# Performance work log

Measured on AMD Instinct MI355X. Metric: run time of the kernel, lower is better.

Reference implementation:

```python
import jax, jax.numpy as jnp
from jax import lax
import numpy as np

D = 256   # d_model
NL = 5    # n_levels
NH = 8    # n_heads
NP = 4    # n_points
DH = D // NH
D_FFN = 1024


def conv2d(x, w, b, stride=1, pad=0):
    y = lax.conv_general_dilated(x, w, (stride, stride), ((pad, pad), (pad, pad)),
                                 dimension_numbers=('NCHW', 'OIHW', 'NCHW'))
    return y + b[None, :, None, None]


def groupnorm(x, g, b, groups=32, eps=1e-5):
    N, C, H, W = x.shape
    xr = x.reshape(N, groups, C // groups, H, W)
    mu = xr.mean((2, 3, 4), keepdims=True)
    var = xr.var((2, 3, 4), keepdims=True)
    xr = (xr - mu) / jnp.sqrt(var + eps)
    return xr.reshape(N, C, H, W) * g[None, :, None, None] + b[None, :, None, None]


def layernorm(x, g, b, eps=1e-5):
    mu = x.mean(-1, keepdims=True)
    var = x.var(-1, keepdims=True)
    return (x - mu) / jnp.sqrt(var + eps) * g + b


def bilinear_sample(value_l, loc, H, W):
    # value_l: (N, H*W, NH, DH); loc: (N, Lq, NH, NP, 2) normalized to [0,1]
    # matches F.grid_sample(mode='bilinear', padding_mode='zeros', align_corners=False)
    N, Lq, nH, nP, _ = loc.shape
    dh = value_l.shape[-1]
    x = loc[..., 0] * W - 0.5
    y = loc[..., 1] * H - 0.5
    x0 = jnp.floor(x)
    y0 = jnp.floor(y)
    wx = x - x0
    wy = y - y0
    x0i = x0.astype(jnp.int32)
    y0i = y0.astype(jnp.int32)
    vt = value_l.transpose(0, 2, 1, 3)  # (N, NH, HW, DH)

    def corner(ix, iy, w):
        valid = (ix >= 0) & (ix < W) & (iy >= 0) & (iy < H)
        idx = jnp.clip(iy, 0, H - 1) * W + jnp.clip(ix, 0, W - 1)  # (N,Lq,NH,NP)
        idx_t = idx.transpose(0, 2, 1, 3).reshape(N, nH, Lq * nP)
        v = jnp.take_along_axis(vt, idx_t[..., None], axis=2)  # (N,NH,Lq*NP,DH)
        v = v.reshape(N, nH, Lq, nP, dh).transpose(0, 2, 1, 3, 4)
        return v * (w * valid)[..., None]

    return (corner(x0i, y0i, (1 - wx) * (1 - wy))
            + corner(x0i + 1, y0i, wx * (1 - wy))
            + corner(x0i, y0i + 1, (1 - wx) * wy)
            + corner(x0i + 1, y0i + 1, wx * wy))


def msdeform_attn(query, ref_pts, value_in, shapes,
                  W_off, b_off, W_aw, b_aw, W_val, b_val, W_out, b_out):
    N, Lq, _ = query.shape
    value = (value_in @ W_val.T + b_val).reshape(N, -1, NH, DH)
    off = (query @ W_off.T + b_off).reshape(N, Lq, NH, NL, NP, 2)
    aw = jax.nn.softmax((query @ W_aw.T + b_aw).reshape(N, Lq, NH, NL * NP), axis=-1)
    aw = aw.reshape(N, Lq, NH, NL, NP)
    # offset normalizer is (W, H) per level
    norm = jnp.array([[wl, hl] for (hl, wl) in shapes], jnp.float32)
    loc = ref_pts[:, :, None, :, None, :] + off / norm[None, None, None, :, None, :]
    out = jnp.zeros((N, Lq, NH, DH), query.dtype)
    start = 0
    for l, (hl, wl) in enumerate(shapes):
        v = value[:, start:start + hl * wl]
        start += hl * wl
        s = bilinear_sample(v, loc[:, :, :, l], hl, wl)  # (N,Lq,NH,NP,DH)
        out = out + jnp.einsum('nqhpd,nqhp->nqhd', s, aw[:, :, :, l])
    return out.reshape(N, Lq, D) @ W_out.T + b_out


def setup_inputs():
    ks = iter(jax.random.split(jax.random.key(0), 48))
    def nrm(shape, s=1.0):
        return jax.random.normal(next(ks), shape, jnp.float32) * s
    return {
        'x0': nrm((2, 128, 100, 100)),
        'x1': nrm((2, 256, 50, 50)),
        'x2': nrm((2, 512, 25, 25)),
        'x3': nrm((2, 1024, 13, 13)),
        'W_ref': nrm((NL * 2, D), 0.02), 'b_ref': jnp.zeros((NL * 2,), jnp.float32),
        'W_off': nrm((NH * NL * NP * 2, D), 0.02), 'b_off': jnp.zeros((NH * NL * NP * 2,), jnp.float32),
        'W_aw': nrm((NH * NL * NP, D), 0.02), 'b_aw': jnp.zeros((NH * NL * NP,), jnp.float32),
        'W_val': nrm((D, D), 0.02), 'b_val': jnp.zeros((D,), jnp.float32),
        'W_out': nrm((D, D), 0.02), 'b_out': jnp.zeros((D,), jnp.float32),
        'gn_g': jnp.ones((D,), jnp.float32), 'gn_b': jnp.zeros((D,), jnp.float32),
        'Wc1': nrm((256, 128, 1, 1), 0.05), 'bc1': jnp.zeros((256,), jnp.float32),
        'Wc2': nrm((256, 512, 1, 1), 0.05), 'bc2': jnp.zeros((256,), jnp.float32),
        'Wc3': nrm((256, 1024, 1, 1), 0.05), 'bc3': jnp.zeros((256,), jnp.float32),
        'Wc4': nrm((256, 1024, 3, 3), 0.02), 'bc4': jnp.zeros((256,), jnp.float32),
        'Wc11': nrm((128, 256, 1, 1), 0.05), 'bc11': jnp.zeros((128,), jnp.float32),
        'Wc22': nrm((512, 256, 1, 1), 0.05), 'bc22': jnp.zeros((512,), jnp.float32),
        'Wc33': nrm((1024, 256, 1, 1), 0.05), 'bc33': jnp.zeros((1024,), jnp.float32),
        'ln1_g': jnp.ones((D,), jnp.float32), 'ln1_b': jnp.zeros((D,), jnp.float32),
        'W1': nrm((D_FFN, D), 0.02), 'b1f': jnp.zeros((D_FFN,), jnp.float32),
        'W2': nrm((D, D_FFN), 0.02), 'b2f': jnp.zeros((D,), jnp.float32),
        'ln2_g': jnp.ones((D,), jnp.float32), 'ln2_b': jnp.zeros((D,), jnp.float32),
    }


def reference(x0, x1, x2, x3, W_ref, b_ref, W_off, b_off, W_aw, b_aw,
              W_val, b_val, W_out, b_out, gn_g, gn_b,
              Wc1, bc1, Wc2, bc2, Wc3, bc3, Wc4, bc4,
              Wc11, bc11, Wc22, bc22, Wc33, bc33,
              ln1_g, ln1_b, W1, b1f, W2, b2f, ln2_g, ln2_b):
    # eval mode: all dropouts are identity
    srcs = [groupnorm(conv2d(x0, Wc1, bc1), gn_g, gn_b),
            x1,
            groupnorm(conv2d(x2, Wc2, bc2), gn_g, gn_b),
            groupnorm(conv2d(x3, Wc3, bc3), gn_g, gn_b),
            groupnorm(conv2d(x3, Wc4, bc4, stride=2, pad=1), gn_g, gn_b)]
    shapes = [(int(s.shape[2]), int(s.shape[3])) for s in srcs]
    N = x0.shape[0]
    src = jnp.concatenate([s.reshape(N, D, -1).transpose(0, 2, 1) for s in srcs], axis=1)
    L = src.shape[1]
    ref_pts = jax.nn.sigmoid(src @ W_ref.T + b_ref).reshape(N, L, NL, 2)
    attn = msdeform_attn(src, ref_pts, src, shapes,
                         W_off, b_off, W_aw, b_aw, W_val, b_val, W_out, b_out)
    h = layernorm(src + attn, ln1_g, ln1_b)
    ffn = jax.nn.relu(h @ W1.T + b1f) @ W2.T + b2f
    h = layernorm(h + ffn, ln2_g, ln2_b)
    sizes = [hl * wl for (hl, wl) in shapes]
    parts = jnp.split(h, np.cumsum(sizes)[:-1].tolist(), axis=1)
    feats = [p.transpose(0, 2, 1).reshape(N, D, hl, wl) for p, (hl, wl) in zip(parts, shapes)]
    return (conv2d(feats[0], Wc11, bc11), feats[1],
            conv2d(feats[2], Wc22, bc22), conv2d(feats[3], Wc33, bc33))
```

## Files before the change

kernel.cpp:

```cpp
#include <hip/hip_runtime.h>
#include <hip/hip_bf16.h>
#include <hip/hip_fp16.h>

#define LTOT 13343
#define NLQ  26686
#define WS_VALB 27326464
#define WS_R    122969088
#define WS_AW   (WS_R + 17079040)
#define WS_REF  (WS_R + 25618560)

typedef __attribute__((ext_vector_type(8))) short bf16x8;
typedef __attribute__((ext_vector_type(4))) float f32x4;
typedef _Float16 f16x2 __attribute__((ext_vector_type(2)));

__device__ __forceinline__ short f2bs(float x) {
  __hip_bfloat16 h = __float2bfloat16(x);
  return __builtin_bit_cast(short, h);
}
__device__ __forceinline__ float b2f(__hip_bfloat16 x) { return __bfloat162float(x); }
__device__ __forceinline__ unsigned short f2bu(float x) {
  return __builtin_bit_cast(unsigned short, __float2bfloat16(x));
}

__device__ __forceinline__ void gld16(const void* g, void* l) {
  __builtin_amdgcn_global_load_lds(
      (const __attribute__((address_space(1))) void*)g,
      (__attribute__((address_space(3))) void*)l, 16, 0, 0);
}

template<int MT, int AMODE, int EPI, int WMODE>
__global__ __launch_bounds__(256) void mgemm_k(
    const __hip_bfloat16* __restrict__ A, const void* __restrict__ Wv,
    const float* __restrict__ bias, void* __restrict__ outv,
    const __hip_bfloat16* __restrict__ resid,
    const float* __restrict__ lng, const float* __restrict__ lnb,
    int M, int Nc, int K, int k_len,
    int A_HW, int A_L, int A_off,
    int O_HW, int O_L, int O_off)
{
  constexpr int NT = (EPI == 9) ? 256 : 128;
  constexpr int JF = (MT == 128 || EPI == 9) ? 4 : 2;
  constexpr bool FAST = (AMODE == 0 && WMODE == 0);
  constexpr int AK = FAST ? 64 : 32;
  constexpr int PA = MT * 32;
  constexpr int PB = NT * 32;
  __shared__ __hip_bfloat16 ldsA[MT * AK];
  __shared__ __hip_bfloat16 ldsB[NT * AK];
  const int t = threadIdx.x;
  const int bm = blockIdx.x * MT, bn = blockIdx.y * NT;
  const int k0 = blockIdx.z * k_len;

  const int sl = t & 63;
  const int mloc = sl & 15;
  const int kbase = (sl >> 4) * 8;
  const int s0 = t >> 6;

  const int r0 = bm + s0 * 16 + mloc, r1 = r0 + 64;
  const int nc0 = bn + s0 * 16 + mloc, nc1 = nc0 + 64;
  const int nc2 = nc0 + 128, nc3 = nc0 + 192;

  const __hip_bfloat16 *ap0 = A, *ap1 = A;
  bool av0 = false, av1 = false;
  int g0n=0, g0h=0, g0w=0, g1n=0, g1h=0, g1w=0;
  if (AMODE == 0) {
    if (r0 < M) { int nn = r0 / A_HW, p = r0 - nn * A_HW;
      ap0 = A + (size_t)(nn * A_L + A_off + p) * K + kbase; av0 = true; }
    if (MT == 128 && r1 < M) { int nn = r1 / A_HW, p = r1 - nn * A_HW;
      ap1 = A + (size_t)(nn * A_L + A_off + p) * K + kbase; av1 = true; }
  } else {
    if (r0 < M) { g0n = r0 / 49; int p = r0 - g0n * 49; g0h = p / 7; g0w = p - g0h * 7; av0 = true; }
    if (r1 < M) { g1n = r1 / 49; int p = r1 - g1n * 49; g1h = p / 7; g1w = p - g1h * 7; av1 = true; }
  }
  const bool wv0 = nc0 < Nc, wv1 = nc1 < Nc;
  const bool wv2 = (EPI == 9) && (nc2 < Nc), wv3 = (EPI == 9) && (nc3 < Nc);
  const __hip_bfloat16 *wb0 = (const __hip_bfloat16*)Wv, *wb1 = wb0, *wb2 = wb0, *wb3 = wb0;
  const float *wf0 = (const float*)Wv, *wf1 = wf0;
  if (WMODE == 0) {
    if (wv0) wb0 = (const __hip_bfloat16*)Wv + (size_t)nc0 * K + kbase;
    if (wv1) wb1 = (const __hip_bfloat16*)Wv + (size_t)nc1 * K + kbase;
    if (wv2) wb2 = (const __hip_bfloat16*)Wv + (size_t)nc2 * K + kbase;
    if (wv3) wb3 = (const __hip_bfloat16*)Wv + (size_t)nc3 * K + kbase;
  } else {
    if (wv0) wf0 = (const float*)Wv + (size_t)nc0 * 9216;
    if (wv1) wf1 = (const float*)Wv + (size_t)nc1 * 9216;
  }

  __hip_bfloat16* lbA0 = ldsA + s0 * 512;
  __hip_bfloat16* lbA1 = lbA0 + 2048;
  __hip_bfloat16* lbB0 = ldsB + s0 * 512;
  __hip_bfloat16* lbB1 = lbB0 + 2048;
  __hip_bfloat16* lbB2 = lbB0 + 4096;
  __hip_bfloat16* lbB3 = lbB0 + 6144;
  __hip_bfloat16* lwA0 = ldsA + s0 * 512 + sl * 8;
  __hip_bfloat16* lwA1 = lwA0 + 2048;
  __hip_bfloat16* lwB0 = ldsB + s0 * 512 + sl * 8;
  __hip_bfloat16* lwB1 = lwB0 + 2048;

  const int lane = t & 63, wv_ = t >> 6;
  const __hip_bfloat16 *rA, *rB;
  int wmR, colbase;
  if (MT == 128) {
    int wm = wv_ >> 1, wn = wv_ & 1;
    rA = ldsA + wm * 2048 + lane * 8;
    rB = ldsB + wn * 2048 + lane * 8;
    wmR = wm * 64;
    colbase = bn + wn * 64;
  } else if (EPI == 9) {
    rA = ldsA + lane * 8;
    rB = ldsB + wv_ * 2048 + lane * 8;
    wmR = 0;
    colbase = bn + wv_ * 64;
  } else {
    rA = ldsA + lane * 8;
    rB = ldsB + wv_ * 1024 + lane * 8;
    wmR = 0;
    colbase = bn + wv_ * 32;
  }

  f32x4 acc[4][JF] = {};

  if (FAST) {
    for (int kt = k0; kt < k0 + k_len; kt += 64) {
      if (av0) { gld16(ap0 + kt, lbA0); gld16(ap0 + kt + 32, lbA0 + PA); }
      if (MT == 128) {
        if (av1) { gld16(ap1 + kt, lbA1); gld16(ap1 + kt + 32, lbA1 + PA); }
      }
      if (wv0) { gld16(wb0 + kt, lbB0); gld16(wb0 + kt + 32, lbB0 + PB); }
      if (wv1) { gld16(wb1 + kt, lbB1); gld16(wb1 + kt + 32, lbB1 + PB); }
      if (EPI == 9) {
        if (wv2) { gld16(wb2 + kt, lbB2); gld16(wb2 + kt + 32, lbB2 + PB); }
        if (wv3) { gld16(wb3 + kt, lbB3); gld16(wb3 + kt + 32, lbB3 + PB); }
      }
      __syncthreads();
#pragma unroll
      for (int h = 0; h < 2; h++) {
        bf16x8 af[4], bfr[JF];
#pragma unroll
        for (int i = 0; i < 4; i++) af[i] = *(const bf16x8*)(rA + h * PA + i * 512);
#pragma unroll
        for (int j = 0; j < JF; j++) bfr[j] = *(const bf16x8*)(rB + h * PB + j * 512);
#pragma unroll
        for (int i = 0; i < 4; i++)
#pragma unroll
          for (int j = 0; j < JF; j++)
            acc[i][j] = __builtin_amdgcn_mfma_f32_16x16x32_bf16(af[i], bfr[j], acc[i][j], 0, 0, 0);
      }
      __syncthreads();
    }
  } else {
    for (int kt = k0; kt < k0 + k_len; kt += 32) {
      {
        bf16x8 va0 = {}, va1 = {};
        int kp = kt + kbase;
        int rs = kp >> 10, c = kp & 1023;
        int rr = rs / 3, ss = rs - rr * 3;
        if (av0) { int ih = g0h*2-1+rr, iw = g0w*2-1+ss;
          if ((unsigned)ih < 13u && (unsigned)iw < 13u)
            va0 = *(const bf16x8*)(A + ((size_t)(g0n*169 + ih*13 + iw))*1024 + c); }
        if (av1) { int ih = g1h*2-1+rr, iw = g1w*2-1+ss;
          if ((unsigned)ih < 13u && (unsigned)iw < 13u)
            va1 = *(const bf16x8*)(A + ((size_t)(g1n*169 + ih*13 + iw))*1024 + c); }
        *(bf16x8*)lwA0 = va0;  *(bf16x8*)lwA1 = va1;
      }
      {
        bf16x8 vb0 = {}, vb1 = {};
        int kp = kt + kbase;
        int rs = kp >> 10, c = kp & 1023;
        if (wv0) { const float* p = wf0 + (size_t)c * 9 + rs;
#pragma unroll
          for (int j = 0; j < 8; j++) vb0[j] = f2bs(p[j * 9]); }
        if (wv1) { const float* p = wf1 + (size_t)c * 9 + rs;
#pragma unroll
          for (int j = 0; j < 8; j++) vb1[j] = f2bs(p[j * 9]); }
        *(bf16x8*)lwB0 = vb0;  *(bf16x8*)lwB1 = vb1;
      }
      __syncthreads();
      bf16x8 af[4], bfr[JF];
#pragma unroll
      for (int i = 0; i < 4; i++) af[i] = *(const bf16x8*)(rA + i * 512);
#pragma unroll
      for (int j = 0; j < JF; j++) bfr[j] = *(const bf16x8*)(rB + j * 512);
#pragma unroll
      for (int i = 0; i < 4; i++)
#pragma unroll
        for (int j = 0; j < JF; j++)
          acc[i][j] = __builtin_amdgcn_mfma_f32_16x16x32_bf16(af[i], bfr[j], acc[i][j], 0, 0, 0);
      __syncthreads();
    }
  }

  const int quad = lane >> 4, nl = lane & 15;

  if constexpr (EPI == 9) {
    float* red  = (float*)ldsB;
    float* redm = (float*)ldsB + 600;
    float bv9[4], gj[4], bj[4]; int cj9[4];
#pragma unroll
    for (int j = 0; j < 4; j++) {
      cj9[j] = colbase + j * 16 + nl;
      bv9[j] = bias[cj9[j]];
      gj[j]  = lng[cj9[j]];
      bj[j]  = lnb[cj9[j]];
    }
#pragma unroll
    for (int i = 0; i < 4; i++) {
#pragma unroll
      for (int r = 0; r < 4; r++) {
        int row64 = i * 16 + quad * 4 + r;
        int m = bm + row64;
        if (m < M) {
          int n = m / O_HW, p = m - n * O_HW;
          size_t orow = (size_t)(n * O_L + O_off + p);
#pragma unroll
          for (int j = 0; j < 4; j++) {
            float v = acc[i][j][r] + bv9[j] + b2f(resid[orow * Nc + cj9[j]]);
            acc[i][j][r] = b2f(__float2bfloat16(v));
          }
        } else {
#pragma unroll
          for (int j = 0; j < 4; j++) acc[i][j][r] = 0.f;
        }
        float s  = acc[i][0][r] + acc[i][1][r] + acc[i][2][r] + acc[i][3][r];
        float s2 = acc[i][0][r]*acc[i][0][r] + acc[i][1][r]*acc[i][1][r]
                 + acc[i][2][r]*acc[i][2][r] + acc[i][3][r]*acc[i][3][r];
        s  += __shfl_xor(s, 1, 64);  s2 += __shfl_xor(s2, 1, 64);
        s  += __shfl_xor(s, 2, 64);  s2 += __shfl_xor(s2, 2, 64);
        s  += __shfl_xor(s, 4, 64);  s2 += __shfl_xor(s2, 4, 64);
        s  += __shfl_xor(s, 8, 64);  s2 += __shfl_xor(s2, 8, 64);
        if (nl == 0) { red[row64 * 9 + wv_ * 2] = s; red[row64 * 9 + wv_ * 2 + 1] = s2; }
      }
    }
    __syncthreads();
    if (t < 64) {
      float S = 0.f, S2 = 0.f;
#pragma unroll
      for (int w = 0; w < 4; w++) { S += red[t * 9 + w * 2]; S2 += red[t * 9 + w * 2 + 1]; }
      float mean = S * (1.f / 256.f);
      float var  = S2 * (1.f / 256.f) - mean * mean;
      redm[t * 2]     = mean;
      redm[t * 2 + 1] = rsqrtf(var + 1e-5f);
    }
    __syncthreads();
#pragma unroll
    for (int i = 0; i < 4; i++) {
#pragma unroll
      for (int r = 0; r < 4; r++) {
        int row64 = i * 16 + quad * 4 + r;
        int m = bm + row64;
        if (m >= M) continue;
        float mean = redm[row64 * 2], rstd = redm[row64 * 2 + 1];
        int n = m / O_HW, p = m - n * O_HW;
        size_t orow = (size_t)(n * O_L + O_off + p);
#pragma unroll
        for (int j = 0; j < 4; j++) {
          float o = (acc[i][j][r] - mean) * rstd * gj[j] + bj[j];
          ((__hip_bfloat16*)outv)[orow * Nc + cj9[j]] = __float2bfloat16(o);
        }
      }
    }
    return;
  }

  float bv[JF]; int cj[JF]; bool cv[JF];
#pragma unroll
  for (int j = 0; j < JF; j++) {
    cj[j] = colbase + j * 16 + nl;
    cv[j] = cj[j] < Nc;
    bv[j] = (EPI != 3 && cv[j]) ? bias[cj[j]] : 0.f;
  }
#pragma unroll
  for (int i = 0; i < 4; i++) {
#pragma unroll
    for (int r = 0; r < 4; r++) {
      int m = bm + wmR + i * 16 + quad * 4 + r;
      if (m >= M) continue;
      int n = m / O_HW, p = m - n * O_HW;
      size_t orow = (size_t)(n * O_L + O_off + p);
#pragma unroll
      for (int j = 0; j < JF; j++) {
        if (!cv[j]) continue;
        float v = acc[i][j][r] + bv[j];
        if (EPI == 1) v = 1.f / (1.f + expf(-v));
        if (EPI == 2) v = fmaxf(v, 0.f);
        if (EPI == 0 || EPI == 1) ((float*)outv)[orow * Nc + cj[j]] = v;
        else if (EPI == 2 || EPI == 6) ((__hip_bfloat16*)outv)[orow * Nc + cj[j]] = __float2bfloat16(v);
        else if (EPI == 3) atomicAdd((float*)outv + orow * Nc + cj[j], acc[i][j][r]);
        else if (EPI == 8) {
          float rv = b2f(resid[orow * Nc + cj[j]]);
          ((__hip_bfloat16*)outv)[orow * Nc + cj[j]] = __float2bfloat16(v + rv);
        }
        else if (EPI == 7) {
          char* base = (char*)outv;
          int q = m, c = cj[j];
          if (c < 256)
            ((_Float16*)(base + WS_VALB))[(size_t)q * 256 + c] = (_Float16)v;
          else if (c < 576)
            ((_Float16*)(base + WS_R))[(size_t)q * 320 + (c - 256)] = (_Float16)v;
          else if (c < 736)
            ((_Float16*)(base + WS_AW))[(size_t)q * 160 + (c - 576)] = (_Float16)v;
          else {
            float sv = 1.f / (1.f + expf(-v));
            ((float*)(base + WS_REF))[(size_t)q * 10 + (c - 736)] = sv;
          }
        }
        else ((float*)outv)[((size_t)n * Nc + cj[j]) * O_HW + p] = v;
      }
    }
  }
}

struct GJob {
  const __hip_bfloat16* A; const __hip_bfloat16* W;
  const float* bias; float* out;
  int M, Nc, K, A_HW, A_L, A_off, O_HW, O_L, O_off, base, nbx;
};
struct GJobs { GJob j[3]; };

template<int EPI, bool WITHCOPY, bool WITHC4>
__global__ __launch_bounds__(256) void mgemm3_k(GJobs tab, int gend,
    const __hip_bfloat16* __restrict__ cpsrc, float* __restrict__ cpdst,
    const __hip_bfloat16* __restrict__ c4A, const __hip_bfloat16* __restrict__ c4W,
    float* __restrict__ c4out, float* __restrict__ stats)
{
  __shared__ char smem[24576];
  __hip_bfloat16* ldsA = (__hip_bfloat16*)smem;
  __hip_bfloat16* ldsB = (__hip_bfloat16*)(smem + 8192);
  const int t = threadIdx.x;
  const int b = blockIdx.x;

  if (WITHCOPY && b >= gend) {
    int bb = b - gend;
    float (*tile)[33] = (float(*)[33])smem;
    int p0 = (bb % 79) * 32; int r = bb / 79; int c0 = (r & 7) * 32; int n = r >> 3;
    int tx = t & 31, ty = t >> 5;
    for (int i = ty; i < 32; i += 8) {
      int p = p0 + i, c = c0 + tx;
      tile[tx][i] = (p < 2500) ? b2f(cpsrc[((size_t)(n * LTOT + 10000 + p)) * 256 + c]) : 0.f;
    }
    __syncthreads();
    for (int i = ty; i < 32; i += 8) {
      int c = c0 + i, p = p0 + tx;
      if (p < 2500) cpdst[((size_t)n * 256 + c) * 2500 + p] = tile[i][tx];
    }
    return;
  }

  if (WITHC4 && b >= gend) {
    int cb = b - gend;
    int kz = cb >> 2, bx2 = cb & 1, by2 = (cb >> 1) & 1;
    int bm = bx2 * 64, bn = by2 * 128;
    int k0 = kz * 288;
    const int sl = t & 63, mloc = sl & 15, kbase = (sl >> 4) * 8, s0 = t >> 6;
    int r0 = bm + s0 * 16 + mloc;
    bool av0 = r0 < 98;
    int g0n = 0, g0h = 0, g0w = 0;
    if (av0) { g0n = r0 / 49; int p = r0 - g0n * 49; g0h = p / 7; g0w = p - g0h * 7; }
    int nc0 = bn + s0 * 16 + mloc, nc1 = nc0 + 64;
    const __hip_bfloat16* wb0 = c4W + (size_t)nc0 * 9216;
    const __hip_bfloat16* wb1 = c4W + (size_t)nc1 * 9216;
    __hip_bfloat16* lwA0 = ldsA + s0 * 512 + sl * 8;
    __hip_bfloat16* lwB0 = ldsB + s0 * 512 + sl * 8;
    __hip_bfloat16* lwB1 = lwB0 + 2048;
    const int lane = t & 63, wvw = t >> 6;
    const __hip_bfloat16* rA = ldsA + lane * 8;
    const __hip_bfloat16* rB = ldsB + wvw * 1024 + lane * 8;
    const int colbase = bn + wvw * 32;
    f32x4 acc[4][2] = {};
    for (int kt = k0; kt < k0 + 288; kt += 32) {
      int kp = kt + kbase;
      {
        bf16x8 va0 = {};
        int rs = kp >> 10, c = kp & 1023;
        int rr = rs / 3, ss = rs - rr * 3;
        if (av0) { int ih = g0h*2-1+rr, iw = g0w*2-1+ss;
          if ((unsigned)ih < 13u && (unsigned)iw < 13u)
            va0 = *(const bf16x8*)(c4A + ((size_t)(g0n*169 + ih*13 + iw))*1024 + c); }
        *(bf16x8*)lwA0 = va0;
      }
      *(bf16x8*)lwB0 = *(const bf16x8*)(wb0 + kp);
      *(bf16x8*)lwB1 = *(const bf16x8*)(wb1 + kp);
      __syncthreads();
      bf16x8 af[4], bfr[2];
#pragma unroll
      for (int i = 0; i < 4; i++) af[i] = *(const bf16x8*)(rA + i * 512);
#pragma unroll
      for (int j2 = 0; j2 < 2; j2++) bfr[j2] = *(const bf16x8*)(rB + j2 * 512);
#pragma unroll
      for (int i = 0; i < 4; i++)
#pragma unroll
        for (int j2 = 0; j2 < 2; j2++)
          acc[i][j2] = __builtin_amdgcn_mfma_f32_16x16x32_bf16(af[i], bfr[j2], acc[i][j2], 0, 0, 0);
      __syncthreads();
    }
    const int quad = lane >> 4, nl = lane & 15;
#pragma unroll
    for (int i = 0; i < 4; i++) {
#pragma unroll
      for (int r = 0; r < 4; r++) {
        int m = bm + i * 16 + quad * 4 + r;
        if (m >= 98) continue;
        int n = m / 49, p = m - n * 49;
        size_t orow = (size_t)(n * LTOT + 13294 + p);
#pragma unroll
        for (int j2 = 0; j2 < 2; j2++)
          atomicAdd(c4out + orow * 256 + colbase + j2 * 16 + nl, acc[i][j2][r]);
      }
    }
    return;
  }

  const int j = (b >= tab.j[1].base) + (b >= tab.j[2].base);
  const GJob J = tab.j[j];
  const int local = b - J.base;
  const int bx = local % J.nbx, by = local / J.nbx;
  const int bm = bx * 64, bn = by * 128;

  const int sl = t & 63, mloc = sl & 15, kbase = (sl >> 4) * 8, s0 = t >> 6;
  const int r0 = bm + s0 * 16 + mloc;
  const int nc0 = bn + s0 * 16 + mloc, nc1 = nc0 + 64;

  const __hip_bfloat16* ap0 = J.A; bool av0 = false;
  if (r0 < J.M) { int nn = r0 / J.A_HW, p = r0 - nn * J.A_HW;
    ap0 = J.A + (size_t)(nn * J.A_L + J.A_off + p) * J.K + kbase; av0 = true; }
  const bool wv0 = nc0 < J.Nc, wv1 = nc1 < J.Nc;
  const __hip_bfloat16 *wb0 = J.W, *wb1 = J.W;
  if (wv0) wb0 = J.W + (size_t)nc0 * J.K + kbase;
  if (wv1) wb1 = J.W + (size_t)nc1 * J.K + kbase;

  __hip_bfloat16* lbA0 = ldsA + s0 * 512;
  __hip_bfloat16* lbB0 = ldsB + s0 * 512;
  __hip_bfloat16* lbB1 = lbB0 + 2048;
  const int lane = t & 63, wv_ = t >> 6;
  const __hip_bfloat16* rA = ldsA + lane * 8;
  const __hip_bfloat16* rB = ldsB + wv_ * 1024 + lane * 8;
  const int colbase = bn + wv_ * 32;

  f32x4 acc[4][2] = {};
  for (int kt = 0; kt < J.K; kt += 64) {
    if (av0) { gld16(ap0 + kt, lbA0); gld16(ap0 + kt + 32, lbA0 + 2048); }
    if (wv0) { gld16(wb0 + kt, lbB0); gld16(wb0 + kt + 32, lbB0 + 4096); }
    if (wv1) { gld16(wb1 + kt, lbB1); gld16(wb1 + kt + 32, lbB1 + 4096); }
    __syncthreads();
#pragma unroll
    for (int h = 0; h < 2; h++) {
      bf16x8 af[4], bfr[2];
#pragma unroll
      for (int i = 0; i < 4; i++) af[i] = *(const bf16x8*)(rA + h * 2048 + i * 512);
#pragma unroll
      for (int j2 = 0; j2 < 2; j2++) bfr[j2] = *(const bf16x8*)(rB + h * 4096 + j2 * 512);
#pragma unroll
      for (int i = 0; i < 4; i++)
#pragma unroll
        for (int j2 = 0; j2 < 2; j2++)
          acc[i][j2] = __builtin_amdgcn_mfma_f32_16x16x32_bf16(af[i], bfr[j2], acc[i][j2], 0, 0, 0);
    }
    __syncthreads();
  }

  const int quad = lane >> 4, nl = lane & 15;
  float bv[2]; int cj[2];
#pragma unroll
  for (int j2 = 0; j2 < 2; j2++) {
    cj[j2] = colbase + j2 * 16 + nl;
    bv[j2] = J.bias[cj[j2]];
  }

  if constexpr (EPI == 0) {
    float sA[2] = {0.f, 0.f}, qA[2] = {0.f, 0.f};
    float sB[2] = {0.f, 0.f}, qB[2] = {0.f, 0.f};
#pragma unroll
    for (int i = 0; i < 4; i++) {
#pragma unroll
      for (int r = 0; r < 4; r++) {
        int m = bm + i * 16 + quad * 4 + r;
        if (m >= J.M) continue;
        int n = m / J.O_HW, p = m - n * J.O_HW;
        size_t orow = (size_t)(n * J.O_L + J.O_off + p);
#pragma unroll
        for (int j2 = 0; j2 < 2; j2++) {
          float v = acc[i][j2][r] + bv[j2];
          J.out[orow * J.Nc + cj[j2]] = v;
          if (n == 0) { sA[j2] += v; qA[j2] += v * v; }
          else        { sB[j2] += v; qB[j2] += v * v; }
        }
      }
    }
    const int msks[5] = {1, 2, 4, 16, 32};
#pragma unroll
    for (int j2 = 0; j2 < 2; j2++) {
      float s0v = sA[j2], q0v = qA[j2], s1v = sB[j2], q1v = qB[j2];
#pragma unroll
      for (int d = 0; d < 5; d++) {
        int msk = msks[d];
        s0v += __shfl_xor(s0v, msk, 64);  q0v += __shfl_xor(q0v, msk, 64);
        s1v += __shfl_xor(s1v, msk, 64);  q1v += __shfl_xor(q1v, msk, 64);
      }
      if (lane == 0 || lane == 8) {
        int g = cj[j2] >> 3;
        if (s0v != 0.f || q0v != 0.f) {
          int si = (j * 2 + 0) * 32 + g;
          atomicAdd(&stats[si * 2], s0v);  atomicAdd(&stats[si * 2 + 1], q0v);
        }
        if (s1v != 0.f || q1v != 0.f) {
          int si = (j * 2 + 1) * 32 + g;
          atomicAdd(&stats[si * 2], s1v);  atomicAdd(&stats[si * 2 + 1], q1v);
        }
      }
    }
    return;
  }

  float* tbuf = (float*)smem;
#pragma unroll
  for (int h2 = 0; h2 < 2; h2++) {
    __syncthreads();
    if ((wv_ >> 1) == h2) {
      int cbase = (wv_ & 1) * 32;
#pragma unroll
      for (int i = 0; i < 4; i++)
#pragma unroll
        for (int r = 0; r < 4; r++) {
          int pl = i * 16 + quad * 4 + r;
#pragma unroll
          for (int j2 = 0; j2 < 2; j2++)
            tbuf[pl * 65 + cbase + j2 * 16 + nl] = acc[i][j2][r] + bv[j2];
        }
    }
    __syncthreads();
#pragma unroll
    for (int kk = 0; kk < 16; kk++) {
      int idx = kk * 256 + t;
      int cl = idx >> 6, pl = idx & 63;
      int m = bm + pl;
      if (m < J.M) {
        int n = m / J.O_HW, p = m - n * J.O_HW;
        J.out[((size_t)n * J.Nc + (bn + h2 * 64 + cl)) * J.O_HW + p] = tbuf[pl * 65 + cl];
      }
    }
  }
}

#define CVT_T13 1632768
struct CvtEnt { const float* s; __hip_bfloat16* d; int n; int base; };
struct CvtTab { CvtEnt e[13]; };
__global__ __launch_bounds__(256) void cvt_weights_k(CvtTab tab,
    const float* __restrict__ bv, const float* __restrict__ bo,
    const float* __restrict__ ba, const float* __restrict__ br,
    float* __restrict__ catbias, float* __restrict__ stats,
    float* __restrict__ src, const float* __restrict__ bc4,
    const float* __restrict__ Wc4f, __hip_bfloat16* __restrict__ wt4)
{
  int i = blockIdx.x * 256 + threadIdx.x;
  if (i < CVT_T13) {
#pragma unroll
    for (int j = 12; j >= 0; j--) {
      if (i >= tab.e[j].base) {
        int k = i - tab.e[j].base;
        tab.e[j].d[k] = __float2bfloat16(tab.e[j].s[k]);
        return;
      }
    }
    return;
  }
  int i2 = i - CVT_T13;
  if (i2 < 1024) {
    if (i2 < 746) {
      float v;
      if (i2 < 256) v = bv[i2];
      else if (i2 < 576) v = bo[i2 - 256];
      else if (i2 < 736) v = ba[i2 - 576];
      else v = br[i2 - 736];
      catbias[i2] = v;
    }
    if (i2 < 512) stats[i2] = 0.f;
    return;
  }
  i2 -= 1024;
  if (i2 < 25088) {
    int blk = i2 >> 8, c = i2 & 255;
    int n = blk / 49, p = blk - n * 49;
    src[((size_t)(n * LTOT + 13294 + p)) * 256 + c] = bc4[c];
    return;
  }
  i2 -= 25088;
  if (i2 < 262144) {
    int nc = i2 >> 10, c = i2 & 1023;
    const float* s = Wc4f + (size_t)nc * 9216 + (size_t)c * 9;
    __hip_bfloat16* d = wt4 + (size_t)nc * 9216 + c;
#pragma unroll
    for (int rs = 0; rs < 9; rs++) d[rs * 1024] = __float2bfloat16(s[rs]);
  }
}

__global__ __launch_bounds__(256) void transpose_all_k(
    const float* __restrict__ x0, const float* __restrict__ x2,
    const float* __restrict__ x3, const float* __restrict__ x1,
    __hip_bfloat16* __restrict__ xt0, __hip_bfloat16* __restrict__ xt2,
    __hip_bfloat16* __restrict__ xt3, __hip_bfloat16* __restrict__ srcb)
{
  __shared__ float tile[32][33];
  int b = blockIdx.x;
  const float* x; __hip_bfloat16* xt; int C, HW, gx, gy, n, lvl1 = 0;
  if (b < 2504)      { x = x0; xt = xt0; C = 128;  HW = 10000; gx = b % 313; int r = b / 313; gy = r & 3; n = r >> 2; }
  else if (b < 3144) { int bb = b - 2504; x = x2; xt = xt2; C = 512;  HW = 625; gx = bb % 20; int r = bb / 20; gy = r & 15; n = r >> 4; }
  else if (b < 3528) { int bb = b - 3144; x = x3; xt = xt3; C = 1024; HW = 169; gx = bb % 6;  int r = bb / 6;  gy = r & 31; n = r >> 5; }
  else               { int bb = b - 3528; x = x1; xt = srcb; C = 256; HW = 2500; gx = bb % 79; int r = bb / 79; gy = r & 7; n = r >> 3; lvl1 = 1; }
  int p0 = gx * 32, c0 = gy * 32;
  const float* xb = x + (size_t)n * C * HW;
  __hip_bfloat16* xtb = lvl1 ? (srcb + ((size_t)(n * LTOT + 10000)) * 256)
                             : (xt + (size_t)n * HW * C);
  int tx = threadIdx.x & 31, ty = threadIdx.x >> 5;
  for (int i = ty; i < 32; i += 8) {
    int c = c0 + i, p = p0 + tx;
    tile[i][tx] = (p < HW) ? xb[(size_t)c * HW + p] : 0.f;
  }
  __syncthreads();
  for (int i = ty; i < 32; i += 8) {
    int p = p0 + i, c = c0 + tx;
    if (p < HW) xtb[(size_t)p * C + c] = __float2bfloat16(tile[tx][i]);
  }
}

__global__ __launch_bounds__(256) void gn_stats4_k(const float* __restrict__ src,
                                                   float* __restrict__ stats)
{
  int n = blockIdx.x, t = threadIdx.x;
  const float* base = src + ((size_t)(n * LTOT + 13294)) * 256 + t;
  float s = 0.f, s2 = 0.f;
  for (int r = 0; r < 49; r++) {
    float v = base[(size_t)r * 256];
    s += v; s2 += v * v;
  }
  s  += __shfl_down(s, 4, 64);  s2 += __shfl_down(s2, 4, 64);
  s  += __shfl_down(s, 2, 64);  s2 += __shfl_down(s2, 2, 64);
  s  += __shfl_down(s, 1, 64);  s2 += __shfl_down(s2, 1, 64);
  if ((t & 7) == 0) {
    int g = t >> 3;
    int si = (3 * 2 + n) * 32 + g;
    atomicAdd(&stats[si * 2],     s);
    atomicAdd(&stats[si * 2 + 1], s2);
  }
}

__global__ __launch_bounds__(256) void gn_apply_k(const float* __restrict__ src,
    __hip_bfloat16* __restrict__ srcb,
    const float* __restrict__ stats, const float* __restrict__ g,
    const float* __restrict__ b)
{
  int x = blockIdx.x;
  int n = x / 10843, cidx = x - n * 10843;
  int li, off, hw, p;
  if (cidx < 10000)      { li = 0; off = 0;     hw = 10000; p = cidx; }
  else if (cidx < 10625) { li = 1; off = 12500; hw = 625;   p = cidx - 10000; }
  else if (cidx < 10794) { li = 2; off = 13125; hw = 169;   p = cidx - 10625; }
  else                   { li = 3; off = 13294; hw = 49;    p = cidx - 10794; }
  int t = threadIdx.x;
  int si = (li * 2 + n) * 32 + (t >> 3);
  float cnt = (float)(hw * 8);
  float mean = stats[si * 2] / cnt;
  float var = stats[si * 2 + 1] / cnt - mean * mean;
  float rstd = rsqrtf(var + 1e-5f);
  size_t a = ((size_t)(n * LTOT + off + p)) * 256 + t;
  float v = (src[a] - mean) * rstd * g[t] + b[t];
  srcb[a] = __float2bfloat16(v);
}

__global__ __launch_bounds__(256) void msdeform_k(const _Float16* __restrict__ value,
    const _Float16* __restrict__ offb, const _Float16* __restrict__ awb,
    const float* __restrict__ refb, __hip_bfloat16* __restrict__ out)
{
  __shared__ float s_awraw[320];
  __shared__ float s_ref[20];
  __shared__ float s_stat[32];
  __shared__ int4 s_cA[320];
  __shared__ int4 s_cB[320];
  const int t = threadIdx.x;
  const int q0 = blockIdx.x * 2;

  for (int i = t; i < 320; i += 256) {
    int ql = (i >= 160) ? 1 : 0;
    s_awraw[i] = (float)awb[(size_t)(q0 + ql) * 160 + (i - ql * 160)];
  }
  if (t < 20) {
    int ql = (t >= 10) ? 1 : 0;
    s_ref[t] = refb[(size_t)(q0 + ql) * 10 + (t - ql * 10)];
  }
  __syncthreads();

  if (t < 16) {
    const float* p = s_awraw + t * 20;
    float m = p[0];
#pragma unroll
    for (int j = 1; j < 20; j++) m = fmaxf(m, p[j]);
    float s = 0.f;
#pragma unroll
    for (int j = 0; j < 20; j++) s += expf(p[j] - m);
    s_stat[t * 2] = m;
    s_stat[t * 2 + 1] = 1.f / s;
  }
  __syncthreads();

  {
    const int Wl[5]   = {100, 50, 25, 13, 7};
    const int lvlo[5] = {0, 10000, 12500, 13125, 13294};
    for (int i = t; i < 320; i += 256) {
      int ql = (i >= 160) ? 1 : 0;
      int j = i - ql * 160;
      int h = j / 20, pt = j - h * 20;
      int l = pt >> 2;
      int q = q0 + ql;
      int W = Wl[l], lo = lvlo[l];
      float fW = (float)W;
      f16x2 o2h = *(const f16x2*)(offb + (size_t)q * 320 + j * 2);
      float ox = (float)o2h[0], oy = (float)o2h[1];
      int hs = (ql * 8 + h) * 2;
      float wgt = expf(s_awraw[i] - s_stat[hs]) * s_stat[hs + 1];
      float rx = s_ref[ql * 10 + l * 2], ry = s_ref[ql * 10 + l * 2 + 1];
      float x = (rx + ox / fW) * fW - 0.5f;
      float y = (ry + oy / fW) * fW - 0.5f;
      float x0f = floorf(x), y0f = floorf(y);
      float wx = x - x0f, wy = y - y0f;
      int x0 = (int)x0f, y0 = (int)y0f;
      int hb = h * 64;
      auto mk = [&](int ix, int iy, float w) {
        bool v = (ix >= 0) & (ix < W) & (iy >= 0) & (iy < W);
        int cx = min(max(ix, 0), W - 1), cy = min(max(iy, 0), W - 1);
        int off = (lo + cy * W + cx) * 512 + hb;
        float fw = v ? w * wgt : 0.f;
        unsigned hbits = (unsigned)__builtin_bit_cast(unsigned short, (_Float16)fw);
        return make_int2(off, (int)(hbits | (hbits << 16)));
      };
      int2 c00 = mk(x0,     y0,     (1.f - wx) * (1.f - wy));
      int2 c10 = mk(x0 + 1, y0,     wx * (1.f - wy));
      int2 c01 = mk(x0,     y0 + 1, (1.f - wx) * wy);
      int2 c11 = mk(x0 + 1, y0 + 1, wx * wy);
      s_cA[i] = make_int4(c00.x, c00.y, c10.x, c10.y);
      s_cB[i] = make_int4(c01.x, c01.y, c11.x, c11.y);
    }
  }
  __syncthreads();

  const int ql = t >> 7, h = (t >> 4) & 7, c2 = t & 15;
  const int q = q0 + ql;
  const int n = q / LTOT;
  const char* vb = (const char*)value + (size_t)n * LTOT * 512 + c2 * 4;
  f16x2 accA = {0, 0}, accB = {0, 0};
  const int bi = ql * 160 + h * 20;
#pragma unroll 5
  for (int p = 0; p < 20; p++) {
    int4 A = s_cA[bi + p];
    int4 B = s_cB[bi + p];
    {
      f16x2 v2 = __builtin_bit_cast(f16x2, *(const unsigned*)(vb + A.x));
      f16x2 w2 = __builtin_bit_cast(f16x2, (unsigned)A.y);
      accA = w2 * v2 + accA;
    }
    {
      f16x2 v2 = __builtin_bit_cast(f16x2, *(const unsigned*)(vb + A.z));
      f16x2 w2 = __builtin_bit_cast(f16x2, (unsigned)A.w);
      accB = w2 * v2 + accB;
    }
    {
      f16x2 v2 = __builtin_bit_cast(f16x2, *(const unsigned*)(vb + B.x));
      f16x2 w2 = __builtin_bit_cast(f16x2, (unsigned)B.y);
      accA = w2 * v2 + accA;
    }
    {
      f16x2 v2 = __builtin_bit_cast(f16x2, *(const unsigned*)(vb + B.z));
      f16x2 w2 = __builtin_bit_cast(f16x2, (unsigned)B.w);
      accB = w2 * v2 + accB;
    }
  }
  float a0 = (float)accA[0] + (float)accB[0];
  float a1 = (float)accA[1] + (float)accB[1];
  unsigned o0 = (unsigned)f2bu(a0);
  unsigned o1 = (unsigned)f2bu(a1);
  *(unsigned*)((char*)out + ((size_t)q * 256 + h * 32 + c2 * 2) * 2) = (o1 << 16) | o0;
}

extern "C" void kernel_launch(void* const* d_in, const int* in_sizes, int n_in,
                              void* d_out, int out_size, void* d_ws, size_t ws_size,
                              hipStream_t stream)
{
  const float* x0    = (const float*)d_in[0];
  const float* x1    = (const float*)d_in[1];
  const float* x2    = (const float*)d_in[2];
  const float* x3    = (const float*)d_in[3];
  const float* W_ref = (const float*)d_in[4];
  const float* b_ref = (const float*)d_in[5];
  const float* W_off = (const float*)d_in[6];
  const float* b_off = (const float*)d_in[7];
  const float* W_aw  = (const float*)d_in[8];
  const float* b_aw  = (const float*)d_in[9];
  const float* W_val = (const float*)d_in[10];
  const float* b_val = (const float*)d_in[11];
  const float* W_outp= (const float*)d_in[12];
  const float* b_outp= (const float*)d_in[13];
  const float* gn_g  = (const float*)d_in[14];
  const float* gn_b  = (const float*)d_in[15];
  const float* Wc1   = (const float*)d_in[16];
  const float* bc1   = (const float*)d_in[17];
  const float* Wc2   = (const float*)d_in[18];
  const float* bc2   = (const float*)d_in[19];
  const float* Wc3   = (const float*)d_in[20];
  const float* bc3   = (const float*)d_in[21];
  const float* Wc4   = (const float*)d_in[22];
  const float* bc4   = (const float*)d_in[23];
  const float* Wc11  = (const float*)d_in[24];
  const float* bc11  = (const float*)d_in[25];
  const float* Wc22  = (const float*)d_in[26];
  const float* bc22  = (const float*)d_in[27];
  const float* Wc33  = (const float*)d_in[28];
  const float* bc33  = (const float*)d_in[29];
  const float* ln1_g = (const float*)d_in[30];
  const float* ln1_b = (const float*)d_in[31];
  const float* W1    = (const float*)d_in[32];
  const float* b1f   = (const float*)d_in[33];
  const float* W2    = (const float*)d_in[34];
  const float* b2f_  = (const float*)d_in[35];
  const float* ln2_g = (const float*)d_in[36];
  const float* ln2_b = (const float*)d_in[37];

  char* wsb = (char*)d_ws;
  float* src             = (float*)(wsb + 0);
  _Float16* valb         = (_Float16*)(wsb + WS_VALB);
  __hip_bfloat16* h2b    = (__hip_bfloat16*)(wsb + 54652928);
  __hip_bfloat16* srcb   = (__hip_bfloat16*)(wsb + 81979392);
  __hip_bfloat16* h1b    = (__hip_bfloat16*)(wsb + 95642624);
  __hip_bfloat16* sampb  = (__hip_bfloat16*)(wsb + 109305856);
  __hip_bfloat16* midb   = (__hip_bfloat16*)(wsb + WS_R);
  _Float16* offbh        = (_Float16*)(wsb + WS_R);
  _Float16* awbh         = (_Float16*)(wsb + WS_AW);
  float* refb            = (float*)(wsb + WS_REF);
  __hip_bfloat16* xt0    = (__hip_bfloat16*)(wsb + WS_R);
  __hip_bfloat16* xt2    = (__hip_bfloat16*)(wsb + WS_R + 5120000);
  __hip_bfloat16* xt3    = (__hip_bfloat16*)(wsb + WS_R + 6400000);
  __hip_bfloat16* wWc4t  = (__hip_bfloat16*)(wsb + WS_R + 8388608);
  __hip_bfloat16* warena = (__hip_bfloat16*)(wsb + 177622016);
  float* stats           = (float*)(wsb + 180887552);
  float* catbias         = (float*)(wsb + 180889600);
  const size_t needed = 180892672;
  if (ws_size < needed) return;

  __hip_bfloat16* wWproj = warena + 0;
  __hip_bfloat16* wW_val = warena + 0;
  __hip_bfloat16* wW_off = warena + 65536;
  __hip_bfloat16* wW_aw  = warena + 147456;
  __hip_bfloat16* wW_ref = warena + 188416;
  __hip_bfloat16* wW_out = warena + 190976;
  __hip_bfloat16* wW1    = warena + 256512;
  __hip_bfloat16* wW2    = warena + 518656;
  __hip_bfloat16* wWc1   = warena + 780800;
  __hip_bfloat16* wWc2   = warena + 813568;
  __hip_bfloat16* wWc3   = warena + 944640;
  __hip_bfloat16* wWc11  = warena + 1206784;
  __hip_bfloat16* wWc22  = warena + 1239552;
  __hip_bfloat16* wWc33  = warena + 1370624;

  dim3 B(256);

  CvtTab tab = {{
    {W_val, wW_val, 65536, 0},       {W_off, wW_off, 81920, 65536},
    {W_aw,  wW_aw,  40960, 147456},  {W_ref, wW_ref, 2560,  188416},
    {W_outp,wW_out, 65536, 190976},  {W1,    wW1,  262144,  256512},
    {W2,    wW2,  262144,  518656},  {Wc1,   wWc1,  32768,  780800},
    {Wc2,   wWc2, 131072,  813568},  {Wc3,   wWc3, 262144,  944640},
    {Wc11,  wWc11, 32768, 1206784},  {Wc22,  wWc22,131072, 1239552},
    {Wc33,  wWc33,262144, 1370624}
  }};
  cvt_weights_k<<<7504,B,0,stream>>>(tab, b_val, b_off, b_aw, b_ref,
                                     catbias, stats, src, bc4, Wc4, wWc4t);

  transpose_all_k<<<4792,B,0,stream>>>(x0, x2, x3, x1, xt0, xt2, xt3, srcb);

  GJobs injobs = {{
    { xt0, wWc1, bc1, src, 20000, 256, 128,  20000, 0, 0, 10000, LTOT, 0,     0,   313 },
    { xt2, wWc2, bc2, src, 1250,  256, 512,  1250,  0, 0, 625,   LTOT, 12500, 626, 20  },
    { xt3, wWc3, bc3, src, 338,   256, 1024, 338,   0, 0, 169,   LTOT, 13125, 666, 6   }
  }};
  mgemm3_k<0,false,true><<<806,B,0,stream>>>(injobs, 678, nullptr, nullptr,
                                             xt3, wWc4t, src, stats);
  gn_stats4_k<<<2,B,0,stream>>>(src, stats);
  gn_apply_k<<<21686,B,0,stream>>>(src, srcb, stats, gn_g, gn_b);

  mgemm_k<128,0,7,0><<<dim3(209,6),B,0,stream>>>(srcb, wWproj, catbias, d_ws, nullptr, nullptr, nullptr, NLQ,746,256,256, NLQ,0,0, NLQ,0,0);
  msdeform_k<<<13343,B,0,stream>>>(valb, offbh, awbh, refb, sampb);

  mgemm_k<64,0,9,0><<<dim3(417,1),B,0,stream>>>(sampb, wW_out, b_outp, h1b, srcb, ln1_g, ln1_b, NLQ,256,256,256, NLQ,0,0, NLQ,0,0);

  mgemm_k<128,0,2,0><<<dim3(209,8),B,0,stream>>>(h1b,  wW1, b1f,  midb,  nullptr, nullptr, nullptr, NLQ,1024,256,256, NLQ,0,0, NLQ,0,0);
  mgemm_k<64,0,9,0><<<dim3(417,1), B,0,stream>>>(midb, wW2, b2f_, h2b, h1b, ln2_g, ln2_b, NLQ,256,1024,1024, NLQ,0,0, NLQ,0,0);

  float* out = (float*)d_out;
  GJobs outjobs = {{
    { h2b, wWc11, bc11, out,           20000, 128,  256, 10000, LTOT, 0,     10000, 0, 0, 0,   313 },
    { h2b, wWc22, bc22, out + 3840000, 1250,  512,  256, 625,   LTOT, 12500, 625,   0, 0, 313, 20  },
    { h2b, wWc33, bc33, out + 4480000, 338,   1024, 256, 169,   LTOT, 13125, 169,   0, 0, 393, 6   }
  }};
  mgemm3_k<4,true,false><<<1705,B,0,stream>>>(outjobs, 441, h2b, out + 2560000,
                                              nullptr, nullptr, nullptr, nullptr);
}
```

Before: 497.4 us.

## Fuse FFN GEMMs, ReLU, residual and LayerNorm into one kernel

Replaces the two FFN GEMM launches with a single kernel. Each 64-row block keeps its h1 tile in LDS and computes the 1024-wide hidden activation in 128-column chunks held in LDS. Each chunk is multiplied immediately by the matching W2 slice, and the kernel finishes with bias, residual and LayerNorm. This removes the global write and read of the large intermediate activation and one launch. In exchange it uses 64KB of LDS per block with only 417 blocks, so occupancy is low, and weight loads are synchronous with no double buffering.

```diff
diff --git a/kernel.cpp b/kernel.cpp
--- a/kernel.cpp
+++ b/kernel.cpp
@@ -304,6 +304,176 @@
           }
         }
         else ((float*)outv)[((size_t)n * Nc + cj[j]) * O_HW + p] = v;
+      }
+    }
+  }
+}
+
+__global__ __launch_bounds__(256) void ffn_k(
+    const __hip_bfloat16* __restrict__ h1, const __hip_bfloat16* __restrict__ W1,
+    const float* __restrict__ b1, const __hip_bfloat16* __restrict__ W2,
+    const float* __restrict__ b2, const float* __restrict__ lng,
+    const float* __restrict__ lnb, __hip_bfloat16* __restrict__ out)
+{
+  __shared__ char smem[65536];
+  __hip_bfloat16* ldsA = (__hip_bfloat16*)smem;
+  __hip_bfloat16* ldsM = (__hip_bfloat16*)(smem + 32768);
+  __hip_bfloat16* ldsW = (__hip_bfloat16*)(smem + 49152);
+  const int t = threadIdx.x;
+  const int bm = blockIdx.x * 64;
+  const int sl = t & 63, mloc = sl & 15, kbase = (sl >> 4) * 8, s0 = t >> 6;
+  const int lane = t & 63, wv_ = t >> 6;
+  const int quad = lane >> 4, nl = lane & 15;
+
+  const int r0 = bm + s0 * 16 + mloc;
+  if (r0 < NLQ) {
+    const __hip_bfloat16* ap = h1 + (size_t)r0 * 256 + kbase;
+#pragma unroll
+    for (int p = 0; p < 4; p++) {
+      gld16(ap + p * 64,      ldsA + p * 4096 + s0 * 512);
+      gld16(ap + p * 64 + 32, ldsA + p * 4096 + s0 * 512 + 2048);
+    }
+  }
+
+  const int ca = s0 * 16 + mloc;
+  const __hip_bfloat16* rA = ldsA + lane * 8;
+  const __hip_bfloat16* rM = ldsM + lane * 8;
+  const __hip_bfloat16* rB = ldsW + wv_ * 1024 + lane * 8;
+
+  f32x4 acc2[4][4] = {};
+
+  for (int c = 0; c < 8; c++) {
+    f32x4 acc1[4][2] = {};
+    const __hip_bfloat16* wp0 = W1 + (size_t)(c * 128 + ca) * 256 + kbase;
+    const __hip_bfloat16* wp1 = wp0 + (size_t)64 * 256;
+    for (int kt = 0; kt < 256; kt += 64) {
+      gld16(wp0 + kt,      ldsW + s0 * 512);
+      gld16(wp0 + kt + 32, ldsW + s0 * 512 + 4096);
+      gld16(wp1 + kt,      ldsW + s0 * 512 + 2048);
+      gld16(wp1 + kt + 32, ldsW + s0 * 512 + 2048 + 4096);
+      __syncthreads();
+      const int p = kt >> 6;
+#pragma unroll
+      for (int h = 0; h < 2; h++) {
+        bf16x8 af[4], bfr[2];
+#pragma unroll
+        for (int i = 0; i < 4; i++) af[i] = *(const bf16x8*)(rA + p * 4096 + h * 2048 + i * 512);
+#pragma unroll
+        for (int j = 0; j < 2; j++) bfr[j] = *(const bf16x8*)(rB + h * 4096 + j * 512);
+#pragma unroll
+        for (int i = 0; i < 4; i++)
+#pragma unroll
+          for (int j = 0; j < 2; j++)
+            acc1[i][j] = __builtin_amdgcn_mfma_f32_16x16x32_bf16(af[i], bfr[j], acc1[i][j], 0, 0, 0);
+      }
+      __syncthreads();
+    }
+#pragma unroll
+    for (int j = 0; j < 2; j++) {
+      int kc = wv_ * 32 + j * 16 + nl;
+      float bb = b1[c * 128 + kc];
+      int ka = (kc >> 6) * 4096 + ((kc >> 5) & 1) * 2048 + ((kc >> 3) & 3) * 128 + (kc & 7);
+#pragma unroll
+      for (int i = 0; i < 4; i++)
+#pragma unroll
+        for (int r = 0; r < 4; r++) {
+          float v = fmaxf(acc1[i][j][r] + bb, 0.f);
+          ldsM[ka + i * 512 + (quad * 4 + r) * 8] = __float2bfloat16(v);
+        }
+    }
+    for (int kt2 = 0; kt2 < 128; kt2 += 64) {
+      const int p2 = kt2 >> 6;
+#pragma unroll
+      for (int hc = 0; hc < 2; hc++) {
+        const __hip_bfloat16* wq0 = W2 + (size_t)(hc * 128 + ca) * 1024 + c * 128 + kt2 + kbase;
+        const __hip_bfloat16* wq1 = wq0 + (size_t)64 * 1024;
+        gld16(wq0,      ldsW + s0 * 512);
+        gld16(wq0 + 32, ldsW + s0 * 512 + 4096);
+        gld16(wq1,      ldsW + s0 * 512 + 2048);
+        gld16(wq1 + 32, ldsW + s0 * 512 + 2048 + 4096);
+        __syncthreads();
+#pragma unroll
+        for (int h = 0; h < 2; h++) {
+          bf16x8 mf[4], bfr[2];
+#pragma unroll
+          for (int i = 0; i < 4; i++) mf[i] = *(const bf16x8*)(rM + p2 * 4096 + h * 2048 + i * 512);
+#pragma unroll
+          for (int j = 0; j < 2; j++) bfr[j] = *(const bf16x8*)(rB + h * 4096 + j * 512);
+#pragma unroll
+          for (int i = 0; i < 4; i++)
+#pragma unroll
+            for (int j = 0; j < 2; j++)
+              acc2[i][hc * 2 + j] = __builtin_amdgcn_mfma_f32_16x16x32_bf16(mf[i], bfr[j], acc2[i][hc * 2 + j], 0, 0, 0);
+        }
+        __syncthreads();
+      }
+    }
+  }
+
+  float* red  = (float*)ldsM;
+  float* redm = (float*)ldsM + 600;
+  float bv9[4], gj[4], bj[4]; int cj9[4];
+#pragma unroll
+  for (int j = 0; j < 4; j++) {
+    int hc = j >> 1, jj = j & 1;
+    cj9[j] = hc * 128 + wv_ * 32 + jj * 16 + nl;
+    bv9[j] = b2[cj9[j]];
+    gj[j]  = lng[cj9[j]];
+    bj[j]  = lnb[cj9[j]];
+  }
+#pragma unroll
+  for (int i = 0; i < 4; i++) {
+#pragma unroll
+    for (int r = 0; r < 4; r++) {
+      int row64 = i * 16 + quad * 4 + r;
+      int m = bm + row64;
+      if (m < NLQ) {
+#pragma unroll
+        for (int j = 0; j < 4; j++) {
+          int k = cj9[j];
+          int la = (k >> 6) * 4096 + ((k >> 5) & 1) * 2048 + i * 512
+                 + ((k >> 3) & 3) * 128 + (quad * 4 + r) * 8 + (k & 7);
+          float rv = b2f(ldsA[la]);
+          float v = acc2[i][j][r] + bv9[j] + rv;
+          acc2[i][j][r] = b2f(__float2bfloat16(v));
+        }
+      } else {
+#pragma unroll
+        for (int j = 0; j < 4; j++) acc2[i][j][r] = 0.f;
+      }
+      float s  = acc2[i][0][r] + acc2[i][1][r] + acc2[i][2][r] + acc2[i][3][r];
+      float s2 = acc2[i][0][r]*acc2[i][0][r] + acc2[i][1][r]*acc2[i][1][r]
+               + acc2[i][2][r]*acc2[i][2][r] + acc2[i][3][r]*acc2[i][3][r];
+      s  += __shfl_xor(s, 1, 64);  s2 += __shfl_xor(s2, 1, 64);
+      s  += __shfl_xor(s, 2, 64);  s2 += __shfl_xor(s2, 2, 64);
+      s  += __shfl_xor(s, 4, 64);  s2 += __shfl_xor(s2, 4, 64);
+      s  += __shfl_xor(s, 8, 64);  s2 += __shfl_xor(s2, 8, 64);
+      if (nl == 0) { red[row64 * 9 + wv_ * 2] = s; red[row64 * 9 + wv_ * 2 + 1] = s2; }
+    }
+  }
+  __syncthreads();
+  if (t < 64) {
+    float S = 0.f, S2 = 0.f;
+#pragma unroll
+    for (int w = 0; w < 4; w++) { S += red[t * 9 + w * 2]; S2 += red[t * 9 + w * 2 + 1]; }
+    float mean = S * (1.f / 256.f);
+    float var  = S2 * (1.f / 256.f) - mean * mean;
+    redm[t * 2]     = mean;
+    redm[t * 2 + 1] = rsqrtf(var + 1e-5f);
+  }
+  __syncthreads();
+#pragma unroll
+  for (int i = 0; i < 4; i++) {
+#pragma unroll
+    for (int r = 0; r < 4; r++) {
+      int row64 = i * 16 + quad * 4 + r;
+      int m = bm + row64;
+      if (m >= NLQ) continue;
+      float mean = redm[row64 * 2], rstd = redm[row64 * 2 + 1];
+#pragma unroll
+      for (int j = 0; j < 4; j++) {
+        float o = (acc2[i][j][r] - mean) * rstd * gj[j] + bj[j];
+        out[(size_t)m * 256 + cj9[j]] = __float2bfloat16(o);
       }
     }
   }
@@ -828,7 +998,6 @@
   __hip_bfloat16* srcb   = (__hip_bfloat16*)(wsb + 81979392);
   __hip_bfloat16* h1b    = (__hip_bfloat16*)(wsb + 95642624);
   __hip_bfloat16* sampb  = (__hip_bfloat16*)(wsb + 109305856);
-  __hip_bfloat16* midb   = (__hip_bfloat16*)(wsb + WS_R);
   _Float16* offbh        = (_Float16*)(wsb + WS_R);
   _Float16* awbh         = (_Float16*)(wsb + WS_AW);
   float* refb            = (float*)(wsb + WS_REF);
@@ -888,8 +1057,7 @@
 
   mgemm_k<64,0,9,0><<<dim3(417,1),B,0,stream>>>(sampb, wW_out, b_outp, h1b, srcb, ln1_g, ln1_b, NLQ,256,256,256, NLQ,0,0, NLQ,0,0);
 
-  mgemm_k<128,0,2,0><<<dim3(209,8),B,0,stream>>>(h1b,  wW1, b1f,  midb,  nullptr, nullptr, nullptr, NLQ,1024,256,256, NLQ,0,0, NLQ,0,0);
-  mgemm_k<64,0,9,0><<<dim3(417,1), B,0,stream>>>(midb, wW2, b2f_, h2b, h1b, ln2_g, ln2_b, NLQ,256,1024,1024, NLQ,0,0, NLQ,0,0);
+  ffn_k<<<417,B,0,stream>>>(h1b, wW1, b1f, wW2, b2f_, ln2_g, ln2_b, h2b);
 
   float* out = (float*)d_out;
   GJobs outjobs = {{
```

Result: faster. 460.5 us, median of 2 (-7.4%).
